# Kernel tuning notes

Measured on AMD Instinct MI355X. Metric: run time of the kernel, lower is better.

The kernel has to match this reference:

```python
import jax, jax.numpy as jnp
import numpy as np

B, T, NC, D = 8, 4096, 2048, 1024  # batch, original_len, num_chunks, d_model


def setup_inputs() -> dict:
    key = jax.random.key(0)
    k1, k2, k3 = jax.random.split(key, 3)
    z = jax.random.normal(k1, (B, NC, D), dtype=jnp.float32)
    p = jax.random.uniform(k2, (B, T), dtype=jnp.float32)
    b = jax.random.randint(k3, (B, T), 0, 2, dtype=jnp.int32)
    return {"z": z, "p": p, "b": b, "original_len": T}


def reference(z, p, b, original_len):
    # z: [B, NC, D], p: [B, T], b: [B, T] boundary flags in {0,1}
    num_chunks = z.shape[1]
    # idx at time t = exclusive cumsum of b (idx advances AFTER copying z[idx]);
    # once idx >= num_chunks the torch loop uses z[:, -1], i.e. clamp to NC-1.
    idx = jnp.clip(jnp.cumsum(b, axis=1) - b, 0, num_chunks - 1)  # [B, T]
    upsampled = jnp.take_along_axis(z, idx[..., None], axis=1)    # [B, T, D]
    coef = p[..., None]                                           # [B, T, 1]
    rolled = jnp.roll(upsampled, shift=1, axis=1)
    smoothed = coef * upsampled + (1.0 - coef) * rolled
    smoothed = smoothed.at[:, 0].set(upsampled[:, 0])
    return smoothed
```

## Files before the change

kernel.cpp:

```cpp
#include <hip/hip_runtime.h>

#define BATCH 8
#define TLEN  4096
#define NCHUNK 2048
#define DMODEL 1024
#define ROWS_PER_BLOCK 16

__global__ void dechunk_scan_kernel(const int* __restrict__ bflag,
                                    int* __restrict__ idx) {
    const int batch = blockIdx.x;
    const int tid = threadIdx.x;
    const int lane = tid & 63;
    const int wid = tid >> 6;
    const int* bb = bflag + (size_t)batch * TLEN;
    int* ii = idx + (size_t)batch * TLEN;

    const int base = tid * 16;
    int vals[16];
    int s = 0;
    const int4* bv = (const int4*)(bb + base);
#pragma unroll
    for (int k = 0; k < 4; ++k) {
        int4 v = bv[k];
        vals[4 * k + 0] = v.x; vals[4 * k + 1] = v.y;
        vals[4 * k + 2] = v.z; vals[4 * k + 3] = v.w;
        s += v.x + v.y + v.z + v.w;
    }

    int incl = s;
#pragma unroll
    for (int off = 1; off < 64; off <<= 1) {
        int n = __shfl_up(incl, off, 64);
        if (lane >= off) incl += n;
    }

    __shared__ int wsum[4];
    if (lane == 63) wsum[wid] = incl;
    __syncthreads();
    int woff = 0;
#pragma unroll
    for (int w = 0; w < 4; ++w)
        woff += (w < wid) ? wsum[w] : 0;

    int run = woff + incl - s;

    int outv[16];
#pragma unroll
    for (int k = 0; k < 16; ++k) {
        outv[k] = min(run, NCHUNK - 1);
        run += vals[k];
    }
    int4* iv = (int4*)(ii + base);
#pragma unroll
    for (int k = 0; k < 4; ++k) {
        iv[k] = make_int4(outv[4 * k + 0], outv[4 * k + 1],
                          outv[4 * k + 2], outv[4 * k + 3]);
    }
}

__global__ void dechunk_smooth_kernel(const float* __restrict__ z,
                                      const float* __restrict__ p,
                                      const int* __restrict__ idx,
                                      float* __restrict__ out) {
    const int chunks_per_batch = TLEN / ROWS_PER_BLOCK;
    const int chunk = blockIdx.x;
    const int batch = chunk / chunks_per_batch;
    const int t0 = (chunk - batch * chunks_per_batch) * ROWS_PER_BLOCK;
    const int tid = threadIdx.x;
    const int bt0 = batch * TLEN + t0;

    __shared__ int lidx[ROWS_PER_BLOCK + 1];
    __shared__ float lp[ROWS_PER_BLOCK];
    if (tid < ROWS_PER_BLOCK + 1) {
        int g = bt0 - 1 + tid;
        lidx[tid] = idx[max(g, 0)];
    } else if (tid >= 32 && tid < 32 + ROWS_PER_BLOCK) {
        lp[tid - 32] = p[bt0 + (tid - 32)];
    }
    __syncthreads();

    const float* zb = z + (size_t)batch * NCHUNK * DMODEL;
    float4* outr = (float4*)(out + (size_t)bt0 * DMODEL);

    float4 v[ROWS_PER_BLOCK + 1];
#pragma unroll
    for (int j = 0; j <= ROWS_PER_BLOCK; ++j) {
        v[j] = ((const float4*)(zb + (size_t)lidx[j] * DMODEL))[tid];
    }

#pragma unroll
    for (int j = 0; j < ROWS_PER_BLOCK; ++j) {
        float4 a = v[j + 1];
        float4 o;
        if (j == 0 && t0 == 0) {
            o = a;
        } else {
            float4 r = v[j];
            const float pv = lp[j];
            const float q = 1.0f - pv;
            o.x = pv * a.x + q * r.x;
            o.y = pv * a.y + q * r.y;
            o.z = pv * a.z + q * r.z;
            o.w = pv * a.w + q * r.w;
        }
        outr[j * (DMODEL / 4) + tid] = o;
    }
}

extern "C" void kernel_launch(void* const* d_in, const int* in_sizes, int n_in,
                              void* d_out, int out_size, void* d_ws, size_t ws_size,
                              hipStream_t stream) {
    const float* z = (const float*)d_in[0];
    const float* p = (const float*)d_in[1];
    const int* bflag = (const int*)d_in[2];
    float* out = (float*)d_out;
    int* idx = (int*)d_ws;

    dechunk_scan_kernel<<<BATCH, 256, 0, stream>>>(bflag, idx);
    dechunk_smooth_kernel<<<BATCH * (TLEN / ROWS_PER_BLOCK), 256, 0, stream>>>(
        z, p, idx, out);
}
```

Measured before the change: 41.44 us.

## Fuse prefix-scan into smoothing kernel by recomputing per-block prefix sums

Removes the separate scan kernel and its workspace round trip. Each smoothing block now recomputes the exclusive prefix of the boundary flags up to its start by reducing the earlier flags of its batch row, then resolves the 17 indices it needs locally. This saves a kernel launch and a serial dependency between the two launches. The cost is redundant reading of up to 4096 flags per block and an extra barrier.

```diff
diff --git a/kernel.cpp b/kernel.cpp
--- a/kernel.cpp
+++ b/kernel.cpp
@@ -6,76 +6,56 @@
 #define DMODEL 1024
 #define ROWS_PER_BLOCK 16
 
-__global__ void dechunk_scan_kernel(const int* __restrict__ bflag,
-                                    int* __restrict__ idx) {
-    const int batch = blockIdx.x;
-    const int tid = threadIdx.x;
-    const int lane = tid & 63;
-    const int wid = tid >> 6;
-    const int* bb = bflag + (size_t)batch * TLEN;
-    int* ii = idx + (size_t)batch * TLEN;
-
-    const int base = tid * 16;
-    int vals[16];
-    int s = 0;
-    const int4* bv = (const int4*)(bb + base);
-#pragma unroll
-    for (int k = 0; k < 4; ++k) {
-        int4 v = bv[k];
-        vals[4 * k + 0] = v.x; vals[4 * k + 1] = v.y;
-        vals[4 * k + 2] = v.z; vals[4 * k + 3] = v.w;
-        s += v.x + v.y + v.z + v.w;
-    }
-
-    int incl = s;
-#pragma unroll
-    for (int off = 1; off < 64; off <<= 1) {
-        int n = __shfl_up(incl, off, 64);
-        if (lane >= off) incl += n;
-    }
-
-    __shared__ int wsum[4];
-    if (lane == 63) wsum[wid] = incl;
-    __syncthreads();
-    int woff = 0;
-#pragma unroll
-    for (int w = 0; w < 4; ++w)
-        woff += (w < wid) ? wsum[w] : 0;
-
-    int run = woff + incl - s;
-
-    int outv[16];
-#pragma unroll
-    for (int k = 0; k < 16; ++k) {
-        outv[k] = min(run, NCHUNK - 1);
-        run += vals[k];
-    }
-    int4* iv = (int4*)(ii + base);
-#pragma unroll
-    for (int k = 0; k < 4; ++k) {
-        iv[k] = make_int4(outv[4 * k + 0], outv[4 * k + 1],
-                          outv[4 * k + 2], outv[4 * k + 3]);
-    }
-}
-
-__global__ void dechunk_smooth_kernel(const float* __restrict__ z,
-                                      const float* __restrict__ p,
-                                      const int* __restrict__ idx,
-                                      float* __restrict__ out) {
+__global__ void dechunk_fused_kernel(const float* __restrict__ z,
+                                     const float* __restrict__ p,
+                                     const int* __restrict__ bflag,
+                                     float* __restrict__ out) {
     const int chunks_per_batch = TLEN / ROWS_PER_BLOCK;
     const int chunk = blockIdx.x;
     const int batch = chunk / chunks_per_batch;
     const int t0 = (chunk - batch * chunks_per_batch) * ROWS_PER_BLOCK;
     const int tid = threadIdx.x;
+    const int lane = tid & 63;
+    const int wid = tid >> 6;
     const int bt0 = batch * TLEN + t0;
+    const int* bb = bflag + (size_t)batch * TLEN;
 
+    __shared__ int wsum[4];
+    __shared__ int wlds[ROWS_PER_BLOCK + 1];
     __shared__ int lidx[ROWS_PER_BLOCK + 1];
     __shared__ float lp[ROWS_PER_BLOCK];
+
+    const int limit = t0 - 1;
+    int s = 0;
+    const int eu = tid * 16;
+    if (eu < limit) {
+        const int4* bv4 = (const int4*)(bb + eu);
+#pragma unroll
+        for (int k = 0; k < 4; ++k) {
+            int4 v = bv4[k];
+            const int u = eu + 4 * k;
+            s += (u + 0 < limit) ? v.x : 0;
+            s += (u + 1 < limit) ? v.y : 0;
+            s += (u + 2 < limit) ? v.z : 0;
+            s += (u + 3 < limit) ? v.w : 0;
+        }
+    }
+#pragma unroll
+    for (int off = 32; off > 0; off >>= 1)
+        s += __shfl_xor(s, off, 64);
+    if (lane == 0) wsum[wid] = s;
+
     if (tid < ROWS_PER_BLOCK + 1) {
-        int g = bt0 - 1 + tid;
-        lidx[tid] = idx[max(g, 0)];
+        wlds[tid] = (t0 == 0 && tid == 0) ? 0 : bb[t0 - 1 + tid];
     } else if (tid >= 32 && tid < 32 + ROWS_PER_BLOCK) {
         lp[tid - 32] = p[bt0 + (tid - 32)];
+    }
+    __syncthreads();
+
+    if (tid < ROWS_PER_BLOCK + 1) {
+        int e = wsum[0] + wsum[1] + wsum[2] + wsum[3];
+        for (int u = 0; u < tid; ++u) e += wlds[u];
+        lidx[tid] = min(e, NCHUNK - 1);
     }
     __syncthreads();
 
@@ -114,9 +94,7 @@
     const float* p = (const float*)d_in[1];
     const int* bflag = (const int*)d_in[2];
     float* out = (float*)d_out;
-    int* idx = (int*)d_ws;
 
-    dechunk_scan_kernel<<<BATCH, 256, 0, stream>>>(bflag, idx);
-    dechunk_smooth_kernel<<<BATCH * (TLEN / ROWS_PER_BLOCK), 256, 0, stream>>>(
-        z, p, idx, out);
+    dechunk_fused_kernel<<<BATCH * (TLEN / ROWS_PER_BLOCK), 256, 0, stream>>>(
+        z, p, bflag, out);
 }
```

After: 37.47 us. -9.6%, faster.
